# Performance work log

Hardware: AMD Instinct MI355X
Metric: run time of the kernel (lower is better)

## Reference

```python
import math
import jax, jax.numpy as jnp
import numpy as np

FACTOR = 2  # init kwarg of AutoCorrelation


def setup_inputs() -> dict:
    key0 = jax.random.key(0)
    kq, kk, kv = jax.random.split(key0, 3)
    B, H, L, D = 8, 8, 2048, 64
    return {
        "query": jax.random.normal(kq, (B, H, L, D), dtype=jnp.float32),
        "key": jax.random.normal(kk, (B, H, L, D), dtype=jnp.float32),
        "value": jax.random.normal(kv, (B, H, L, D), dtype=jnp.float32),
    }


def reference(query, key, value):
    # Inference (eval-mode) path of AutoCorrelation.forward.
    B, H, L, D = query.shape
    L_KV = key.shape[2]
    # _pad_or_truncate_key_value: match key/value length to query length
    if L > L_KV:
        pad = [(0, 0), (0, 0), (0, L - L_KV), (0, 0)]
        key = jnp.pad(key, pad)
        value = jnp.pad(value, pad)
    else:
        key = key[:, :, :L, :]
        value = value[:, :, :L, :]

    # _period_based_dependency: circular cross-correlation via FFT
    qf = jnp.fft.rfft(jnp.swapaxes(query, -2, -1), axis=-1)   # (B,H,D,L//2+1) complex
    kf = jnp.fft.rfft(jnp.swapaxes(key, -2, -1), axis=-1)
    corr = jnp.fft.irfft(qf * jnp.conj(kf), n=L, axis=-1)     # (B,H,D,L)

    # _time_delay_aggregation (eval branch: per-batch topk delays)
    mean_corr = corr.mean(axis=(1, 2))                         # (B,L)
    num_delays = min(FACTOR * math.ceil(math.log(L)), L)
    w, delay_idx = jax.lax.top_k(mean_corr, num_delays)       # (B,k)
    w = jax.nn.softmax(w, axis=-1)

    ar = jnp.arange(L)

    def body(ctx, inp):
        d, wk = inp  # (B,), (B,)
        idx = (ar[None, :] + d[:, None]) % L                   # (B,L) — circular shift == gather from doubled value
        gathered = jnp.take_along_axis(
            value, jnp.broadcast_to(idx[:, None, :, None], value.shape), axis=2
        )                                                      # (B,H,L,D)
        return ctx + wk[:, None, None, None] * gathered, None

    ctx0 = jnp.zeros_like(value)
    context, _ = jax.lax.scan(body, ctx0, (delay_idx.T, w.T))
    return context
```

## Files before the change

kernel.cpp:

```cpp
#include <hip/hip_runtime.h>

static constexpr int LSEQ = 2048;
static constexpr int NB   = 8;
static constexpr int NH   = 8;
static constexpr int ND   = 64;
static constexpr int NDEL = 16;

static constexpr size_t WS_P_OFF     = 0;
static constexpr size_t WS_W_OFF     = 8388608;
static constexpr size_t WS_DELAY_OFF = 8389120;

__device__ __forceinline__ int SWZ(int x) { return x ^ (((x >> 4) & 7) << 1); }

__device__ __forceinline__ int pof(int f) {
    return ((f & 7) << 8) | (((f >> 3) & 7) << 5) | (((f >> 6) & 7) << 2) | (f >> 9);
}
__device__ __forceinline__ int fofp(int p) {
    return (p >> 8) | (((p >> 5) & 7) << 3) | (((p >> 2) & 7) << 6) | ((p & 3) << 9);
}

#define CMUL(ar, ai, br, bi) make_float2((ar)*(br) - (ai)*(bi), (ar)*(bi) + (ai)*(br))

__device__ __forceinline__ void dft8(const float2 x[8], float2 X[8]) {
    const float RH = 0.70710678118654752440f;
    float2 a0 = make_float2(x[0].x + x[4].x, x[0].y + x[4].y);
    float2 a1 = make_float2(x[1].x + x[5].x, x[1].y + x[5].y);
    float2 a2 = make_float2(x[2].x + x[6].x, x[2].y + x[6].y);
    float2 a3 = make_float2(x[3].x + x[7].x, x[3].y + x[7].y);
    float2 b0 = make_float2(x[0].x - x[4].x, x[0].y - x[4].y);
    float  t1r = x[1].x - x[5].x, t1i = x[1].y - x[5].y;
    float2 b1 = make_float2(RH * (t1r + t1i), RH * (t1i - t1r));
    float  t2r = x[2].x - x[6].x, t2i = x[2].y - x[6].y;
    float2 b2 = make_float2(t2i, -t2r);
    float  t3r = x[3].x - x[7].x, t3i = x[3].y - x[7].y;
    float2 b3 = make_float2(RH * (t3i - t3r), -RH * (t3r + t3i));
    float2 c0 = make_float2(a0.x + a2.x, a0.y + a2.y);
    float2 d0 = make_float2(a0.x - a2.x, a0.y - a2.y);
    float2 c1 = make_float2(a1.x + a3.x, a1.y + a3.y);
    float2 d1 = make_float2(a1.y - a3.y, -(a1.x - a3.x));
    X[0] = make_float2(c0.x + c1.x, c0.y + c1.y);
    X[4] = make_float2(c0.x - c1.x, c0.y - c1.y);
    X[2] = make_float2(d0.x + d1.x, d0.y + d1.y);
    X[6] = make_float2(d0.x - d1.x, d0.y - d1.y);
    float2 e0 = make_float2(b0.x + b2.x, b0.y + b2.y);
    float2 f0 = make_float2(b0.x - b2.x, b0.y - b2.y);
    float2 e1 = make_float2(b1.x + b3.x, b1.y + b3.y);
    float2 f1 = make_float2(b1.y - b3.y, -(b1.x - b3.x));
    X[1] = make_float2(e0.x + e1.x, e0.y + e1.y);
    X[5] = make_float2(e0.x - e1.x, e0.y - e1.y);
    X[3] = make_float2(f0.x + f1.x, f0.y + f1.y);
    X[7] = make_float2(f0.x - f1.x, f0.y - f1.y);
}

__device__ __forceinline__ void dft4(const float2 x[4], float2 X[4]) {
    float2 s0 = make_float2(x[0].x + x[2].x, x[0].y + x[2].y);
    float2 s1 = make_float2(x[1].x + x[3].x, x[1].y + x[3].y);
    float2 d0 = make_float2(x[0].x - x[2].x, x[0].y - x[2].y);
    float2 d1 = make_float2(x[1].y - x[3].y, -(x[1].x - x[3].x));
    X[0] = make_float2(s0.x + s1.x, s0.y + s1.y);
    X[2] = make_float2(s0.x - s1.x, s0.y - s1.y);
    X[1] = make_float2(d0.x + d1.x, d0.y + d1.y);
    X[3] = make_float2(d0.x - d1.x, d0.y - d1.y);
}

__device__ __forceinline__ void stageR8(float2* zp, const int adr[8], const float2 W[7]) {
    float2 X[8], Y[8];
    #pragma unroll
    for (int j = 0; j < 8; ++j) X[j] = zp[adr[j]];
    dft8(X, Y);
    #pragma unroll
    for (int m = 1; m < 8; ++m) Y[m] = CMUL(Y[m].x, Y[m].y, W[m-1].x, W[m-1].y);
    #pragma unroll
    for (int m = 0; m < 8; ++m) zp[adr[m]] = Y[m];
}

__device__ __forceinline__ void stageD(float2* zp, const int adr[8], float2 X[8]) {
    float2 xin[8];
    #pragma unroll
    for (int j = 0; j < 8; ++j) xin[j] = zp[adr[j]];
    dft4(&xin[0], &X[0]);
    dft4(&xin[4], &X[4]);
    #pragma unroll
    for (int m = 0; m < 8; ++m) zp[adr[m]] = X[m];
}

__global__ __launch_bounds__(256, 2) void fft_corr(const float* __restrict__ q,
                                                   const float* __restrict__ k,
                                                   float2* __restrict__ Pc) {
    __shared__ float2 z0[LSEQ], z1[LSEQ];
    const int t    = threadIdx.x;
    const int bi   = blockIdx.x;
    const int xcd  = bi & 7;
    const int sl   = bi >> 3;
    const int bh   = xcd * 8 + (sl >> 4);
    const int grp  = (sl >> 1) & 7;
    const int half = sl & 1;
    const int b    = bh >> 3;
    const int h    = bh & 7;
    const size_t base = (size_t)bh * LSEQ * ND + (size_t)(grp * 8 + half * 4);

    float2 WA[7], WB[7], WC[7];
    {
        float sn, cs;
        __sincosf(-6.28318530717958647692f * (float)t / 2048.f, &sn, &cs);
        WA[0] = make_float2(cs, sn);
        __sincosf(-6.28318530717958647692f * (float)(t & 31) / 256.f, &sn, &cs);
        WB[0] = make_float2(cs, sn);
        __sincosf(-6.28318530717958647692f * (float)(t & 3) / 32.f, &sn, &cs);
        WC[0] = make_float2(cs, sn);
        #pragma unroll
        for (int m = 1; m < 7; ++m) {
            WA[m] = CMUL(WA[m-1].x, WA[m-1].y, WA[0].x, WA[0].y);
            WB[m] = CMUL(WB[m-1].x, WB[m-1].y, WB[0].x, WB[0].y);
            WC[m] = CMUL(WC[m-1].x, WC[m-1].y, WC[0].x, WC[0].y);
        }
    }

    int fS[4], pmS[4];
    #pragma unroll
    for (int s = 0; s < 4; ++s) {
        const int cc = (s < 2) ? s : s + 2;
        const int f  = fofp(8 * t + cc);
        const int m  = (2048 - f) & 2047;
        fS[s]  = f;
        pmS[s] = SWZ(pof(m));
    }
    float aFr[4] = {0, 0, 0, 0}, aFi[4] = {0, 0, 0, 0};
    float aS = 0.f;

    const int sbB   = (t >> 5) * 256 + (t & 31);
    const int baseC = (t >> 2) * 32 + (t & 3);
    int adrB[8], adrC[8], adrD[8];
    #pragma unroll
    for (int n = 0; n < 8; ++n) {
        adrB[n] = SWZ(sbB + 32 * n);
        adrC[n] = SWZ(baseC + 4 * n);
        adrD[n] = SWZ(8 * t + n);
    }

    float4 qa[8], ka[8];
    #pragma unroll
    for (int j = 0; j < 8; ++j) {
        const size_t r = base + (size_t)(t + 256 * j) * ND;
        qa[j] = *(const float4*)(q + r);
        ka[j] = *(const float4*)(k + r);
    }
    #pragma unroll
    for (int pr = 0; pr < 2; ++pr) {
        const int c0 = 2 * pr, c1 = 2 * pr + 1;
        float2 X0[8], X1[8], Y0[8], Y1[8];
        #pragma unroll
        for (int j = 0; j < 8; ++j) {
            X0[j] = make_float2((&qa[j].x)[c0], (&ka[j].x)[c0]);
            X1[j] = make_float2((&qa[j].x)[c1], (&ka[j].x)[c1]);
        }
        __syncthreads();

        dft8(X0, Y0);
        dft8(X1, Y1);
        #pragma unroll
        for (int m = 1; m < 8; ++m) {
            Y0[m] = CMUL(Y0[m].x, Y0[m].y, WA[m-1].x, WA[m-1].y);
            Y1[m] = CMUL(Y1[m].x, Y1[m].y, WA[m-1].x, WA[m-1].y);
        }
        #pragma unroll
        for (int m = 0; m < 8; ++m) {
            const int a = SWZ(m * 256 + t);
            z0[a] = Y0[m];
            z1[a] = Y1[m];
        }
        __syncthreads();

        stageR8(z0, adrB, WB);
        stageR8(z1, adrB, WB);
        __syncthreads();

        stageR8(z0, adrC, WC);
        stageR8(z1, adrC, WC);
        __syncthreads();

        stageD(z0, adrD, X0);
        stageD(z1, adrD, X1);
        __syncthreads();

        #pragma unroll
        for (int s = 0; s < 4; ++s) {
            const int cc = (s < 2) ? s : s + 2;
            {
                const float2 Zf = X0[cc], Zm = z0[pmS[s]];
                const float qr = 0.5f * (Zf.x + Zm.x), qi = 0.5f * (Zf.y - Zm.y);
                const float kr = 0.5f * (Zf.y + Zm.y), ki = 0.5f * (Zm.x - Zf.x);
                aFr[s] += qr * kr + qi * ki;
                aFi[s] += qi * kr - qr * ki;
            }
            {
                const float2 Zf = X1[cc], Zm = z1[pmS[s]];
                const float qr = 0.5f * (Zf.x + Zm.x), qi = 0.5f * (Zf.y - Zm.y);
                const float kr = 0.5f * (Zf.y + Zm.y), ki = 0.5f * (Zm.x - Zf.x);
                aFr[s] += qr * kr + qi * ki;
                aFi[s] += qi * kr - qr * ki;
            }
        }
        if (t == 0) aS += X0[2].x * X0[2].y + X1[2].x * X1[2].y;
    }

    const int part = h * 16 + grp * 2 + half;
    float2* Pp = Pc + (size_t)part * (NB * 1024) + (size_t)b * 1024;
    #pragma unroll
    for (int s = 0; s < 4; ++s) Pp[fS[s]] = make_float2(aFr[s], aFi[s]);
    if (t == 0) Pp[0] = make_float2(aFr[0], aS);
}

__global__ __launch_bounds__(256) void reduce_S(float2* __restrict__ Pc) {
    const int g = blockIdx.x * 256 + threadIdx.x;
    float ax = 0.f, ay = 0.f;
    #pragma unroll 8
    for (int part = 0; part < 128; ++part) {
        const float2 v = Pc[(size_t)part * (NB * 1024) + g];
        ax += v.x; ay += v.y;
    }
    Pc[g] = make_float2(ax, ay);
}

__global__ __launch_bounds__(256) void ifft_topk(const float2* __restrict__ S,
                                                 float* __restrict__ wout,
                                                 int* __restrict__ dout) {
    __shared__ float2 zz[LSEQ];
    __shared__ float  mc[LSEQ];
    __shared__ float  pv[4];
    __shared__ int    pig[4];
    __shared__ float  topv[NDEL];
    __shared__ int    topi[NDEL];
    const int b = blockIdx.x, t = threadIdx.x;

    float2 WA[7], WB[7], WC[7];
    {
        float sn, cs;
        __sincosf(-6.28318530717958647692f * (float)t / 2048.f, &sn, &cs);
        WA[0] = make_float2(cs, sn);
        __sincosf(-6.28318530717958647692f * (float)(t & 31) / 256.f, &sn, &cs);
        WB[0] = make_float2(cs, sn);
        __sincosf(-6.28318530717958647692f * (float)(t & 3) / 32.f, &sn, &cs);
        WC[0] = make_float2(cs, sn);
        #pragma unroll
        for (int m = 1; m < 7; ++m) {
            WA[m] = CMUL(WA[m-1].x, WA[m-1].y, WA[0].x, WA[0].y);
            WB[m] = CMUL(WB[m-1].x, WB[m-1].y, WB[0].x, WB[0].y);
            WC[m] = CMUL(WC[m-1].x, WC[m-1].y, WC[0].x, WC[0].y);
        }
    }
    const int sbB   = (t >> 5) * 256 + (t & 31);
    const int baseC = (t >> 2) * 32 + (t & 3);
    int adrB[8], adrC[8], adrD[8];
    #pragma unroll
    for (int n = 0; n < 8; ++n) {
        adrB[n] = SWZ(sbB + 32 * n);
        adrC[n] = SWZ(baseC + 4 * n);
        adrD[n] = SWZ(8 * t + n);
    }

    #pragma unroll
    for (int u = 0; u < 4; ++u) {
        const int j = t + 256 * u;
        const float2 s = S[b * 1024 + j];
        if (j == 0) {
            zz[0] = make_float2(s.x, 0.f);
            zz[2] = make_float2(s.y, 0.f);
        } else {
            zz[pof(j)]        = s;
            zz[pof(2048 - j)] = make_float2(s.x, -s.y);
        }
    }
    __syncthreads();

    float2 X[8], Y[8];
    #pragma unroll
    for (int j = 0; j < 8; ++j) {
        const float2 s = zz[pof(t + 256 * j)];
        X[j] = make_float2(s.x, -s.y);
    }
    __syncthreads();

    dft8(X, Y);
    #pragma unroll
    for (int m = 1; m < 8; ++m) Y[m] = CMUL(Y[m].x, Y[m].y, WA[m-1].x, WA[m-1].y);
    #pragma unroll
    for (int m = 0; m < 8; ++m) zz[SWZ(m * 256 + t)] = Y[m];
    __syncthreads();

    stageR8(zz, adrB, WB);
    __syncthreads();
    stageR8(zz, adrC, WC);
    __syncthreads();

    {
        float2 xin[8];
        #pragma unroll
        for (int j = 0; j < 8; ++j) xin[j] = zz[adrD[j]];
        dft4(&xin[0], &X[0]);
        dft4(&xin[4], &X[4]);
    }

    const float scale = 1.0f / ((float)LSEQ * (float)(NH * ND));
    #pragma unroll
    for (int cc = 0; cc < 8; ++cc) mc[fofp(8 * t + cc)] = X[cc].x * scale;
    __syncthreads();

    const int lane = t & 63, wv = t >> 6;
    for (int it = 0; it < NDEL; ++it) {
        float bv = -3e38f; int bix = 0;
        #pragma unroll
        for (int u = 0; u < 8; ++u) {
            const int idx = t + 256 * u;
            const float v = mc[idx];
            if (v > bv || (v == bv && idx < bix)) { bv = v; bix = idx; }
        }
        #pragma unroll
        for (int off = 32; off; off >>= 1) {
            const float ov = __shfl_xor(bv, off);
            const int   oi = __shfl_xor(bix, off);
            if (ov > bv || (ov == bv && oi < bix)) { bv = ov; bix = oi; }
        }
        if (lane == 0) { pv[wv] = bv; pig[wv] = bix; }
        __syncthreads();
        if (t < 64) {
            float v = (t < 4) ? pv[t] : -3e38f;
            int  ii = (t < 4) ? pig[t] : 0;
            #pragma unroll
            for (int off = 2; off; off >>= 1) {
                const float ov = __shfl_xor(v, off);
                const int   oi = __shfl_xor(ii, off);
                if (ov > v || (ov == v && oi < ii)) { v = ov; ii = oi; }
            }
            if (t == 0) { topv[it] = v; topi[it] = ii; mc[ii] = -3e38f; }
        }
        __syncthreads();
    }

    if (t == 0) {
        const float m = topv[0];
        float e[NDEL], sum = 0.f;
        for (int i = 0; i < NDEL; ++i) { e[i] = __expf(topv[i] - m); sum += e[i]; }
        const float inv = 1.0f / sum;
        for (int i = 0; i < NDEL; ++i) {
            wout[b * NDEL + i] = e[i] * inv;
            dout[b * NDEL + i] = topi[i];
        }
    }
}

__global__ __launch_bounds__(256) void gather_out(const float* __restrict__ v,
                                                  const float* __restrict__ w,
                                                  const int* __restrict__ delay,
                                                  float* __restrict__ out) {
    const int bi  = blockIdx.x;
    const int xcd = bi & 7;
    const int s   = bi >> 3;
    const int bh  = xcd * 8 + (s >> 7);
    const int bt  = s & 127;
    const int b   = bh >> 3;
    const int tid = threadIdx.x;

    __shared__ float sw_[NDEL];
    __shared__ int   sd_[NDEL];
    if (tid < NDEL) {
        sw_[tid] = w[b * NDEL + tid];
        sd_[tid] = delay[b * NDEL + tid];
    }
    __syncthreads();

    const float* vb = v + (size_t)bh * LSEQ * ND;
    float*       ob = out + (size_t)bh * LSEQ * ND;

    const int row = tid >> 4;
    const int col = (tid & 15) * 4;
    const int t   = bt * 16 + row;

    float4 acc = make_float4(0.f, 0.f, 0.f, 0.f);
    #pragma unroll
    for (int kk = 0; kk < NDEL; ++kk) {
        const int r = (t + sd_[kk]) & (LSEQ - 1);
        const float4 vv = *(const float4*)(vb + (size_t)r * ND + col);
        const float wv = sw_[kk];
        acc.x += wv * vv.x; acc.y += wv * vv.y;
        acc.z += wv * vv.z; acc.w += wv * vv.w;
    }
    *(float4*)(ob + (size_t)t * ND + col) = acc;
}

extern "C" void kernel_launch(void* const* d_in, const int* in_sizes, int n_in,
                              void* d_out, int out_size, void* d_ws, size_t ws_size,
                              hipStream_t stream) {
    const float* q = (const float*)d_in[0];
    const float* k = (const float*)d_in[1];
    const float* v = (const float*)d_in[2];
    float* out = (float*)d_out;

    float2* Pc    = (float2*)((char*)d_ws + WS_P_OFF);
    float*  w     = (float*)((char*)d_ws + WS_W_OFF);
    int*    delay = (int*)((char*)d_ws + WS_DELAY_OFF);

    fft_corr<<<dim3(1024), dim3(256), 0, stream>>>(q, k, Pc);
    reduce_S<<<dim3(32), dim3(256), 0, stream>>>(Pc);
    ifft_topk<<<dim3(NB), dim3(256), 0, stream>>>(Pc, w, delay);
    gather_out<<<dim3(NB * NH * 128), dim3(256), 0, stream>>>(v, w, delay, out);
}
```

Baseline: 209.4 us.

## Parallelize partial reduction, register-resident top-k, fewer barriers, nontemporal output stores

```diff
diff --git a/kernel.cpp b/kernel.cpp
--- a/kernel.cpp
+++ b/kernel.cpp
@@ -145,17 +145,15 @@
         qa[j] = *(const float4*)(q + r);
         ka[j] = *(const float4*)(k + r);
     }
-    #pragma unroll
-    for (int pr = 0; pr < 2; ++pr) {
-        const int c0 = 2 * pr, c1 = 2 * pr + 1;
-        float2 X0[8], X1[8], Y0[8], Y1[8];
+
+    float2 X0[8], X1[8], Y0[8], Y1[8];
+
+    auto stageA = [&](int c0, int c1) {
         #pragma unroll
         for (int j = 0; j < 8; ++j) {
             X0[j] = make_float2((&qa[j].x)[c0], (&ka[j].x)[c0]);
             X1[j] = make_float2((&qa[j].x)[c1], (&ka[j].x)[c1]);
         }
-        __syncthreads();
-
         dft8(X0, Y0);
         dft8(X1, Y1);
         #pragma unroll
@@ -169,20 +167,16 @@
             z0[a] = Y0[m];
             z1[a] = Y1[m];
         }
-        __syncthreads();
-
+    };
+    auto stageBCD = [&]() {
         stageR8(z0, adrB, WB);
         stageR8(z1, adrB, WB);
-        __syncthreads();
-
         stageR8(z0, adrC, WC);
         stageR8(z1, adrC, WC);
-        __syncthreads();
-
         stageD(z0, adrD, X0);
         stageD(z1, adrD, X1);
-        __syncthreads();
-
+    };
+    auto product = [&]() {
         #pragma unroll
         for (int s = 0; s < 4; ++s) {
             const int cc = (s < 2) ? s : s + 2;
@@ -202,7 +196,19 @@
             }
         }
         if (t == 0) aS += X0[2].x * X0[2].y + X1[2].x * X1[2].y;
-    }
+    };
+
+    stageA(0, 1);
+    __syncthreads();
+    stageBCD();
+    __syncthreads();
+    product();
+    __syncthreads();
+    stageA(2, 3);
+    __syncthreads();
+    stageBCD();
+    __syncthreads();
+    product();
 
     const int part = h * 16 + grp * 2 + half;
     float2* Pp = Pc + (size_t)part * (NB * 1024) + (size_t)b * 1024;
@@ -212,14 +218,25 @@
 }
 
 __global__ __launch_bounds__(256) void reduce_S(float2* __restrict__ Pc) {
-    const int g = blockIdx.x * 256 + threadIdx.x;
+    __shared__ float2 acc[256];
+    const int t     = threadIdx.x;
+    const int bi    = blockIdx.x;
+    const int b     = bi & 7;
+    const int seg   = bi >> 3;
+    const int col   = b * 1024 + seg * 64 + (t & 63);
+    const int slice = t >> 6;
     float ax = 0.f, ay = 0.f;
     #pragma unroll 8
-    for (int part = 0; part < 128; ++part) {
-        const float2 v = Pc[(size_t)part * (NB * 1024) + g];
+    for (int pp = 0; pp < 32; ++pp) {
+        const float2 v = Pc[(size_t)(slice * 32 + pp) * (NB * 1024) + col];
         ax += v.x; ay += v.y;
     }
-    Pc[g] = make_float2(ax, ay);
+    acc[t] = make_float2(ax, ay);
+    __syncthreads();
+    if (t < 64) {
+        const float2 r0 = acc[t], r1 = acc[t + 64], r2 = acc[t + 128], r3 = acc[t + 192];
+        Pc[col] = make_float2(r0.x + r1.x + r2.x + r3.x, r0.y + r1.y + r2.y + r3.y);
+    }
 }
 
 __global__ __launch_bounds__(256) void ifft_topk(const float2* __restrict__ S,
@@ -227,10 +244,8 @@
                                                  int* __restrict__ dout) {
     __shared__ float2 zz[LSEQ];
     __shared__ float  mc[LSEQ];
-    __shared__ float  pv[4];
-    __shared__ int    pig[4];
-    __shared__ float  topv[NDEL];
-    __shared__ int    topi[NDEL];
+    __shared__ float  candv[4][NDEL];
+    __shared__ int    candt[4][NDEL];
     const int b = blockIdx.x, t = threadIdx.x;
 
     float2 WA[7], WB[7], WC[7];
@@ -289,10 +304,7 @@
     __syncthreads();
 
     stageR8(zz, adrB, WB);
-    __syncthreads();
     stageR8(zz, adrC, WC);
-    __syncthreads();
-
     {
         float2 xin[8];
         #pragma unroll
@@ -306,38 +318,42 @@
     for (int cc = 0; cc < 8; ++cc) mc[fofp(8 * t + cc)] = X[cc].x * scale;
     __syncthreads();
 
-    const int lane = t & 63, wv = t >> 6;
+    const int L = t & 63, wv = t >> 6;
+    float v[8];
+    #pragma unroll
+    for (int u = 0; u < 8; ++u) v[u] = mc[512 * wv + 64 * u + L];
+
     for (int it = 0; it < NDEL; ++it) {
-        float bv = -3e38f; int bix = 0;
-        #pragma unroll
-        for (int u = 0; u < 8; ++u) {
-            const int idx = t + 256 * u;
-            const float v = mc[idx];
-            if (v > bv || (v == bv && idx < bix)) { bv = v; bix = idx; }
-        }
+        float bv = v[0]; int bu = 0;
+        #pragma unroll
+        for (int u = 1; u < 8; ++u) if (v[u] > bv) { bv = v[u]; bu = u; }
+        int bt_ = 512 * wv + 64 * bu + L;
         #pragma unroll
         for (int off = 32; off; off >>= 1) {
             const float ov = __shfl_xor(bv, off);
-            const int   oi = __shfl_xor(bix, off);
-            if (ov > bv || (ov == bv && oi < bix)) { bv = ov; bix = oi; }
-        }
-        if (lane == 0) { pv[wv] = bv; pig[wv] = bix; }
-        __syncthreads();
-        if (t < 64) {
-            float v = (t < 4) ? pv[t] : -3e38f;
-            int  ii = (t < 4) ? pig[t] : 0;
+            const int   ot = __shfl_xor(bt_, off);
+            if (ov > bv || (ov == bv && ot < bt_)) { bv = ov; bt_ = ot; }
+        }
+        #pragma unroll
+        for (int u = 0; u < 8; ++u)
+            if (512 * wv + 64 * u + L == bt_) v[u] = -3e38f;
+        if (L == 0) { candv[wv][it] = bv; candt[wv][it] = bt_; }
+    }
+    __syncthreads();
+
+    if (t == 0) {
+        int hp[4] = {0, 0, 0, 0};
+        float topv[NDEL]; int topi[NDEL];
+        for (int it = 0; it < NDEL; ++it) {
+            float bv = -3e38f; int bt_ = 1 << 30; int bw = 0;
             #pragma unroll
-            for (int off = 2; off; off >>= 1) {
-                const float ov = __shfl_xor(v, off);
-                const int   oi = __shfl_xor(ii, off);
-                if (ov > v || (ov == v && oi < ii)) { v = ov; ii = oi; }
+            for (int ww = 0; ww < 4; ++ww) {
+                const float cv = candv[ww][hp[ww]];
+                const int   ct = candt[ww][hp[ww]];
+                if (cv > bv || (cv == bv && ct < bt_)) { bv = cv; bt_ = ct; bw = ww; }
             }
-            if (t == 0) { topv[it] = v; topi[it] = ii; mc[ii] = -3e38f; }
-        }
-        __syncthreads();
-    }
-
-    if (t == 0) {
+            topv[it] = bv; topi[it] = bt_; ++hp[bw];
+        }
         const float m = topv[0];
         float e[NDEL], sum = 0.f;
         for (int i = 0; i < NDEL; ++i) { e[i] = __expf(topv[i] - m); sum += e[i]; }
@@ -348,6 +364,8 @@
         }
     }
 }
+
+typedef float f4nt __attribute__((ext_vector_type(4)));
 
 __global__ __launch_bounds__(256) void gather_out(const float* __restrict__ v,
                                                   const float* __restrict__ w,
@@ -385,7 +403,8 @@
         acc.x += wv * vv.x; acc.y += wv * vv.y;
         acc.z += wv * vv.z; acc.w += wv * vv.w;
     }
-    *(float4*)(ob + (size_t)t * ND + col) = acc;
+    f4nt val = {acc.x, acc.y, acc.z, acc.w};
+    __builtin_nontemporal_store(val, (f4nt*)(ob + (size_t)t * ND + col));
 }
 
 extern "C" void kernel_launch(void* const* d_in, const int* in_sizes, int n_in,
@@ -401,7 +420,7 @@
     int*    delay = (int*)((char*)d_ws + WS_DELAY_OFF);
 
     fft_corr<<<dim3(1024), dim3(256), 0, stream>>>(q, k, Pc);
-    reduce_S<<<dim3(32), dim3(256), 0, stream>>>(Pc);
+    reduce_S<<<dim3(128), dim3(256), 0, stream>>>(Pc);
     ifft_topk<<<dim3(NB), dim3(256), 0, stream>>>(Pc, w, delay);
     gather_out<<<dim3(NB * NH * 128), dim3(256), 0, stream>>>(v, w, delay, out);
 }
```

Measured after the change: 201.2 us. 1.04x faster.
